# Performance work log

Hardware: AMD Instinct MI355X
Metric: run time of the kernel (lower is better)

## Reference

```python
import jax, jax.numpy as jnp
import numpy as np

N_M = 100000  # musicians
N_T = 100000  # tracks
E = 400000
D = 128


def _sage(x_src, x_dst, edge, W_l, b_l, W_r, n_dst):
    """PyG SAGEConv: lin_l(mean_{j in N(i)} x_src[j]) + lin_r(x_dst[i])."""
    src, dst = edge[0], edge[1]
    msg = x_src[src]                                   # [E, D] gather
    agg = jax.ops.segment_sum(msg, dst, num_segments=n_dst)
    cnt = jax.ops.segment_sum(jnp.ones((edge.shape[1],), x_src.dtype), dst,
                              num_segments=n_dst)
    agg = agg / jnp.maximum(cnt, 1.0)[:, None]         # mean aggregation
    return agg @ W_l.T + b_l + x_dst @ W_r.T


def setup_inputs() -> dict:
    key = jax.random.key(0)
    ks = jax.random.split(key, 7)
    scale = 0.05
    return {
        "x_m": jax.random.normal(ks[0], (N_M, D), jnp.float32),
        "x_t": jax.random.normal(ks[1], (N_T, D), jnp.float32),
        "Wl": jax.random.normal(ks[2], (3, 2, D, D), jnp.float32) * scale,
        "bl": jnp.zeros((3, 2, D), jnp.float32),
        "Wr": jax.random.normal(ks[3], (3, 2, D, D), jnp.float32) * scale,
        "edge_mt": jax.random.randint(ks[4], (2, E), 0, N_T, jnp.int32).astype(jnp.int64),
        "edge_tm": jax.random.randint(ks[5], (2, E), 0, N_M, jnp.int32).astype(jnp.int64),
    }


def reference(x_m, x_t, Wl, bl, Wr, edge_mt, edge_tm):
    # 3 HeteroConv(SAGEConv) layers; dropout=0.0 is identity.
    for layer in range(3):
        # edge type 0: musician -plays_on-> track  (dst = track)
        new_t = _sage(x_m, x_t, edge_mt, Wl[layer, 0], bl[layer, 0], Wr[layer, 0], N_T)
        # edge type 1: track -features-> musician  (dst = musician)
        new_m = _sage(x_t, x_m, edge_tm, Wl[layer, 1], bl[layer, 1], Wr[layer, 1], N_M)
        if layer < 2:
            new_m = jax.nn.relu(new_m)
            new_t = jax.nn.relu(new_t)
        x_m, x_t = new_m, new_t
    return x_m, x_t
```

## Files before the change

### kernel.cpp

```cpp
#include <hip/hip_runtime.h>
#include <hip/hip_bf16.h>

typedef __bf16 bf16_t;
typedef __attribute__((ext_vector_type(4))) __bf16 bf16x4;
typedef __attribute__((ext_vector_type(8))) __bf16 bf16x8;
typedef __attribute__((ext_vector_type(4))) float f32x4;

#define DIM 128

__device__ __forceinline__ void gl_lds16(const void* g, void* l) {
    __builtin_amdgcn_global_load_lds(
        (const __attribute__((address_space(1))) unsigned int*)g,
        (__attribute__((address_space(3))) unsigned int*)l, 16, 0, 0);
}

__global__ void prep_count(const float* __restrict__ Wl, const float* __restrict__ Wr,
                           bf16_t* __restrict__ Wc,
                           const int* __restrict__ dA, int* __restrict__ cA,
                           const int* __restrict__ dB, int* __restrict__ cB,
                           int E, int PB) {
    int blk = blockIdx.x;
    if (blk < PB) {
        int idx = blk * 256 + threadIdx.x;
        if (idx >= 6 * 128 * 256) return;
        int k = idx & 255;
        int n = (idx >> 8) & 127;
        int s = idx >> 15;
        float v;
        if (k < 128) v = Wl[((size_t)s * 128 + n) * 128 + k];
        else         v = Wr[((size_t)s * 128 + n) * 128 + (k - 128)];
        Wc[idx] = (bf16_t)v;
    } else {
        int i = (blk - PB) * 256 + threadIdx.x;
        if (i < E) atomicAdd(&cA[dA[i]], 1);
        else if (i < 2 * E) atomicAdd(&cB[dB[i - E]], 1);
    }
}

__global__ __launch_bounds__(256) void scan_local2(
    const int* __restrict__ cntA, int* __restrict__ partA, int* __restrict__ bsumA,
    int MA, int NBA,
    const int* __restrict__ cntB, int* __restrict__ partB, int* __restrict__ bsumB,
    int MB) {
    int blk = blockIdx.x;
    const int* cnt; int* partial; int* blocksum; int M; int b;
    if (blk < NBA) { cnt = cntA; partial = partA; blocksum = bsumA; M = MA; b = blk; }
    else           { cnt = cntB; partial = partB; blocksum = bsumB; M = MB; b = blk - NBA; }
    __shared__ int sdata[256];
    int i = b * 256 + threadIdx.x;
    int v = (i < M) ? cnt[i] : 0;
    sdata[threadIdx.x] = v;
    __syncthreads();
    for (int off = 1; off < 256; off <<= 1) {
        int t = (threadIdx.x >= off) ? sdata[threadIdx.x - off] : 0;
        __syncthreads();
        sdata[threadIdx.x] += t;
        __syncthreads();
    }
    int incl = sdata[threadIdx.x];
    if (i < M) partial[i] = incl - v;
    if (threadIdx.x == 255) blocksum[b] = incl;
}

__global__ __launch_bounds__(256) void scan_blocks2(int* __restrict__ bsA, int NA,
                                                    int* __restrict__ bsB, int NBcnt) {
    int* blocksum = blockIdx.x ? bsB : bsA;
    int NB = blockIdx.x ? NBcnt : NA;
    __shared__ int sdata[256];
    __shared__ int running;
    if (threadIdx.x == 0) running = 0;
    __syncthreads();
    for (int base = 0; base < NB; base += 256) {
        int i = base + threadIdx.x;
        int v = (i < NB) ? blocksum[i] : 0;
        sdata[threadIdx.x] = v;
        __syncthreads();
        for (int off = 1; off < 256; off <<= 1) {
            int t = (threadIdx.x >= off) ? sdata[threadIdx.x - off] : 0;
            __syncthreads();
            sdata[threadIdx.x] += t;
            __syncthreads();
        }
        int incl = sdata[threadIdx.x];
        int r = running;
        __syncthreads();
        if (i < NB) blocksum[i] = incl - v + r;
        if (threadIdx.x == 0) running = r + sdata[255];
        __syncthreads();
    }
}

__global__ __launch_bounds__(256) void add_offsets2(
    const int* __restrict__ pA, const int* __restrict__ bsA,
    int* __restrict__ rsA, int* __restrict__ curA, int MA, int NBA,
    const int* __restrict__ pB, const int* __restrict__ bsB,
    int* __restrict__ rsB, int* __restrict__ curB, int MB) {
    int blk = blockIdx.x;
    const int *partial, *blocksum; int *rowstart, *cursor; int M, b;
    if (blk < NBA) { partial = pA; blocksum = bsA; rowstart = rsA; cursor = curA; M = MA; b = blk; }
    else           { partial = pB; blocksum = bsB; rowstart = rsB; cursor = curB; M = MB; b = blk - NBA; }
    int i = b * 256 + threadIdx.x;
    if (i < M) {
        int rs = partial[i] + blocksum[i >> 8];
        rowstart[i] = rs;
        cursor[i] = rs;
    }
}

__global__ void bin_edges2(const int* __restrict__ sA, const int* __restrict__ dA,
                           int* __restrict__ curA, int* __restrict__ csrA,
                           const int* __restrict__ sB, const int* __restrict__ dB,
                           int* __restrict__ curB, int* __restrict__ csrB, int E) {
    int e = blockIdx.x * blockDim.x + threadIdx.x;
    if (e < E) {
        int d = dA[e];
        int pos = atomicAdd(&curA[d], 1);
        csrA[pos] = sA[e];
    } else if (e < 2 * E) {
        int i = e - E;
        int d = dB[i];
        int pos = atomicAdd(&curB[d], 1);
        csrB[pos] = sB[i];
    }
}

__global__ __launch_bounds__(256) void gather2(
    const float* __restrict__ xsA, const int* __restrict__ rsA,
    const int* __restrict__ cnA, const int* __restrict__ csA,
    bf16_t* __restrict__ agA, int MA,
    const float* __restrict__ xsB, const int* __restrict__ rsB,
    const int* __restrict__ cnB, const int* __restrict__ csB,
    bf16_t* __restrict__ agB, int MB) {
    int gw   = (blockIdx.x * 256 + threadIdx.x) >> 6;
    int lane = threadIdx.x & 63;
    int half = lane >> 5;
    int l32  = lane & 31;
    int side = gw & 1;
    int d    = (gw >> 1) * 2 + half;
    const float* xs; const int *rs, *cn, *cs; bf16_t* ag; int M;
    if (side == 0) { xs = xsA; rs = rsA; cn = cnA; cs = csA; ag = agA; M = MA; }
    else           { xs = xsB; rs = rsB; cn = cnB; cs = csB; ag = agB; M = MB; }
    if (d >= M) return;

    int start = rs[d];
    int n = cn[d];
    float4 acc0 = {0.f, 0.f, 0.f, 0.f};
    float4 acc1 = {0.f, 0.f, 0.f, 0.f};
    for (int k = 0; k < n; k += 8) {
        int sv[8];
#pragma unroll
        for (int j = 0; j < 8; ++j) {
            int kk = k + j;
            sv[j] = cs[start + min(kk, n - 1)];
        }
        float4 vv[8];
#pragma unroll
        for (int j = 0; j < 8; ++j)
            vv[j] = ((const float4*)(xs + (size_t)sv[j] * DIM))[l32];
#pragma unroll
        for (int j = 0; j < 8; j += 2) {
            float w0 = (k + j     < n) ? 1.f : 0.f;
            float w1 = (k + j + 1 < n) ? 1.f : 0.f;
            acc0.x += vv[j].x * w0; acc0.y += vv[j].y * w0;
            acc0.z += vv[j].z * w0; acc0.w += vv[j].w * w0;
            acc1.x += vv[j + 1].x * w1; acc1.y += vv[j + 1].y * w1;
            acc1.z += vv[j + 1].z * w1; acc1.w += vv[j + 1].w * w1;
        }
    }
    float invn = 1.0f / (float)max(n, 1);
    bf16x4 r;
    r[0] = (bf16_t)((acc0.x + acc1.x) * invn);
    r[1] = (bf16_t)((acc0.y + acc1.y) * invn);
    r[2] = (bf16_t)((acc0.z + acc1.z) * invn);
    r[3] = (bf16_t)((acc0.w + acc1.w) * invn);
    *(bf16x4*)(ag + (size_t)d * DIM + l32 * 4) = r;
}

#define GTILE   32
#define A0BYTES 8192
#define A1BYTES 16384
#define LDSBUF  (A0BYTES + A1BYTES)

template <bool RELU>
__global__ __launch_bounds__(256, 3) void gemm2(
    const bf16_t* __restrict__ A0a, const float* __restrict__ A1a,
    const bf16_t* __restrict__ Wca, const float* __restrict__ ba,
    float* __restrict__ oa, int Ma,
    const bf16_t* __restrict__ A0b, const float* __restrict__ A1b,
    const bf16_t* __restrict__ Wcb, const float* __restrict__ bb,
    float* __restrict__ ob, int Mb) {
    __shared__ char smem[2 * LDSBUF];
    const int tid  = threadIdx.x;
    const int wid  = tid >> 6;
    const int lane = tid & 63;
    const int quad = lane >> 4;
    const int l16  = lane & 15;

    const int side = blockIdx.x & 1;
    const int t0   = blockIdx.x >> 1;
    const int gs   = gridDim.x >> 1;

    const bf16_t* A0; const float* A1; const bf16_t* Wc; const float* bias; float* out; int M;
    if (side == 0) { A0 = A0a; A1 = A1a; Wc = Wca; bias = ba; out = oa; M = Ma; }
    else           { A0 = A0b; A1 = A1b; Wc = Wcb; bias = bb; out = ob; M = Mb; }
    const int nt = (M + GTILE - 1) / GTILE;
    if (t0 >= nt) return;

    bf16x8 breg[2][8];
#pragma unroll
    for (int ct = 0; ct < 2; ++ct)
#pragma unroll
        for (int kt = 0; kt < 8; ++kt)
            breg[ct][kt] = *(const bf16x8*)(
                Wc + (size_t)(wid * 32 + ct * 16 + l16) * 256 + kt * 32 + quad * 8);

    const float bcol0 = bias[wid * 32 + l16];
    const float bcol1 = bias[wid * 32 + 16 + l16];
    const int sw = l16 & 7;

    int a0row[2], a0sc[2];
#pragma unroll
    for (int c = 0; c < 2; ++c) {
        int o  = wid * 2048 + c * 1024 + lane * 16;
        int row = o >> 8;
        int ch  = (o >> 4) & 15;
        a0row[c] = row;
        a0sc[c]  = (ch ^ (row & 7)) * 8;
    }
    int a1row[4], a1sc[4];
#pragma unroll
    for (int c = 0; c < 4; ++c) {
        int o  = wid * 4096 + c * 1024 + lane * 16;
        int row = o >> 9;
        int ch  = (o >> 4) & 31;
        a1row[c] = row;
        a1sc[c]  = (ch ^ (row & 7)) * 4;
    }

    auto STAGE = [&](int b, int t) {
        const int r0 = t * GTILE;
        char* base = smem + b * LDSBUF;
#pragma unroll
        for (int c = 0; c < 2; ++c) {
            int grow = r0 + a0row[c]; if (grow >= M) grow = M - 1;
            gl_lds16(A0 + (size_t)grow * DIM + a0sc[c],
                     base + wid * 2048 + c * 1024);
        }
#pragma unroll
        for (int c = 0; c < 4; ++c) {
            int grow = r0 + a1row[c]; if (grow >= M) grow = M - 1;
            gl_lds16(A1 + (size_t)grow * DIM + a1sc[c],
                     base + A0BYTES + wid * 4096 + c * 1024);
        }
    };

    auto COMPUTE = [&](int b, int t) {
        const int r0 = t * GTILE;
        const char* a0base = smem + b * LDSBUF;
        const char* a1base = a0base + A0BYTES;
        f32x4 acc[2][2];
#pragma unroll
        for (int rt = 0; rt < 2; ++rt) {
            acc[rt][0] = (f32x4){0.f, 0.f, 0.f, 0.f};
            acc[rt][1] = (f32x4){0.f, 0.f, 0.f, 0.f};
        }
#pragma unroll
        for (int rt = 0; rt < 2; ++rt) {
            const int row = rt * 16 + l16;
            bf16x8 alo[4];
#pragma unroll
            for (int kt = 0; kt < 4; ++kt)
                alo[kt] = *(const bf16x8*)(a0base + row * 256 + ((kt * 4 + quad) ^ sw) * 16);
#pragma unroll
            for (int kt = 0; kt < 4; ++kt) {
                acc[rt][0] = __builtin_amdgcn_mfma_f32_16x16x32_bf16(alo[kt], breg[0][kt], acc[rt][0], 0, 0, 0);
                acc[rt][1] = __builtin_amdgcn_mfma_f32_16x16x32_bf16(alo[kt], breg[1][kt], acc[rt][1], 0, 0, 0);
            }
#pragma unroll
            for (int kt = 0; kt < 4; ++kt) {
                const int cc = kt * 8 + quad * 2;
                float4 x0 = *(const float4*)(a1base + row * 512 + ((cc)     ^ sw) * 16);
                float4 x1 = *(const float4*)(a1base + row * 512 + ((cc + 1) ^ sw) * 16);
                bf16x8 ah;
                ah[0] = (bf16_t)x0.x; ah[1] = (bf16_t)x0.y;
                ah[2] = (bf16_t)x0.z; ah[3] = (bf16_t)x0.w;
                ah[4] = (bf16_t)x1.x; ah[5] = (bf16_t)x1.y;
                ah[6] = (bf16_t)x1.z; ah[7] = (bf16_t)x1.w;
                acc[rt][0] = __builtin_amdgcn_mfma_f32_16x16x32_bf16(ah, breg[0][kt + 4], acc[rt][0], 0, 0, 0);
                acc[rt][1] = __builtin_amdgcn_mfma_f32_16x16x32_bf16(ah, breg[1][kt + 4], acc[rt][1], 0, 0, 0);
            }
        }
#pragma unroll
        for (int ct = 0; ct < 2; ++ct) {
            const int col = wid * 32 + ct * 16 + l16;
            const float bv = ct ? bcol1 : bcol0;
#pragma unroll
            for (int rt = 0; rt < 2; ++rt)
#pragma unroll
                for (int r = 0; r < 4; ++r) {
                    int row = r0 + rt * 16 + quad * 4 + r;
                    if (row < M) {
                        float v = acc[rt][ct][r] + bv;
                        if (RELU) v = fmaxf(v, 0.f);
                        out[(size_t)row * DIM + col] = v;
                    }
                }
        }
    };

    STAGE(0, t0);
    int bufi = 0;
    for (int t = t0; t < nt; t += gs, bufi ^= 1) {
        const int nxt = t + gs;
        if (nxt < nt) {
            STAGE(bufi ^ 1, nxt);
            asm volatile("s_waitcnt vmcnt(6)" ::: "memory");
        } else {
            asm volatile("s_waitcnt vmcnt(0)" ::: "memory");
        }
        __builtin_amdgcn_s_barrier();
        COMPUTE(bufi, t);
        __builtin_amdgcn_s_barrier();
        __builtin_amdgcn_sched_barrier(0);
    }
}

extern "C" void kernel_launch(void* const* d_in, const int* in_sizes, int n_in,
                              void* d_out, int out_size, void* d_ws, size_t ws_size,
                              hipStream_t stream) {
    const float* x_m = (const float*)d_in[0];
    const float* x_t = (const float*)d_in[1];
    const float* Wl  = (const float*)d_in[2];
    const float* bl  = (const float*)d_in[3];
    const float* Wr  = (const float*)d_in[4];
    const int* e_mt  = (const int*)d_in[5];
    const int* e_tm  = (const int*)d_in[6];

    const int Mm = in_sizes[0] / DIM;
    const int Mt = in_sizes[1] / DIM;
    const int E  = in_sizes[5] / 2;
    const int NBt = (Mt + 255) / 256;
    const int NBm = (Mm + 255) / 256;

    float* out_m = (float*)d_out;
    float* out_t = (float*)d_out + (size_t)Mm * DIM;

    char* ws = (char*)d_ws;
    size_t off = 0;
    auto alloc = [&](size_t bytes) -> void* {
        void* p = ws + off;
        off += (bytes + 255) & ~(size_t)255;
        return p;
    };
    float*  xm2    = (float*)alloc((size_t)Mm * DIM * 4);
    float*  xt2    = (float*)alloc((size_t)Mt * DIM * 4);
    bf16_t* aggT   = (bf16_t*)alloc((size_t)Mt * DIM * 2);
    bf16_t* aggM   = (bf16_t*)alloc((size_t)Mm * DIM * 2);
    int*    cnt_t  = (int*)alloc((size_t)Mt * 4);
    int*    cnt_m  = (int*)alloc((size_t)Mm * 4);
    int*    rs_t   = (int*)alloc((size_t)Mt * 4);
    int*    rs_m   = (int*)alloc((size_t)Mm * 4);
    int*    cur_tb = (int*)alloc((size_t)Mt * 4);
    int*    cur_mb = (int*)alloc((size_t)Mm * 4);
    int*    part_t = (int*)alloc((size_t)Mt * 4);
    int*    part_m = (int*)alloc((size_t)Mm * 4);
    int*    bsum_t = (int*)alloc((size_t)NBt * 4);
    int*    bsum_m = (int*)alloc((size_t)NBm * 4);
    int*    csr_t  = (int*)alloc((size_t)E * 4);
    int*    csr_m  = (int*)alloc((size_t)E * 4);
    bf16_t* Wc     = (bf16_t*)alloc((size_t)6 * 128 * 256 * 2);

    hipMemsetAsync(cnt_t, 0, (size_t)Mt * 4, stream);
    hipMemsetAsync(cnt_m, 0, (size_t)Mm * 4, stream);

    const int PB = (6 * 128 * 256 + 255) / 256;
    const int CB = (2 * E + 255) / 256;
    prep_count<<<PB + CB, 256, 0, stream>>>(Wl, Wr, Wc, e_mt + E, cnt_t, e_tm + E, cnt_m, E, PB);

    scan_local2<<<NBt + NBm, 256, 0, stream>>>(cnt_t, part_t, bsum_t, Mt, NBt,
                                               cnt_m, part_m, bsum_m, Mm);
    scan_blocks2<<<2, 256, 0, stream>>>(bsum_t, NBt, bsum_m, NBm);
    add_offsets2<<<NBt + NBm, 256, 0, stream>>>(part_t, bsum_t, rs_t, cur_tb, Mt, NBt,
                                                part_m, bsum_m, rs_m, cur_mb, Mm);
    bin_edges2<<<(2 * E + 255) / 256, 256, 0, stream>>>(e_mt, e_mt + E, cur_tb, csr_t,
                                                        e_tm, e_tm + E, cur_mb, csr_m, E);

    const int wT = (Mt + 1) / 2, wM = (Mm + 1) / 2;
    const int gwaves = 2 * ((wT > wM) ? wT : wM);
    const int gblocks = (gwaves + 3) / 4;

    int GG = 768;
    {
        int ntT = (Mt + GTILE - 1) / GTILE, ntM = (Mm + GTILE - 1) / GTILE;
        int need = 2 * ((ntT > ntM) ? ntT : ntM);
        if (GG > need) GG = need;
        GG &= ~1;
        if (GG < 2) GG = 2;
    }

    const float* cm = x_m;
    const float* ct = x_t;
    for (int layer = 0; layer < 3; ++layer) {
        float *nxt_m, *nxt_t;
        if (layer == 1) { nxt_m = xm2;   nxt_t = xt2;   }
        else            { nxt_m = out_m; nxt_t = out_t; }
        const float* biasT = bl + ((size_t)layer * 2 + 0) * DIM;
        const float* biasM = bl + ((size_t)layer * 2 + 1) * DIM;
        const bf16_t* WcT = Wc + ((size_t)layer * 2 + 0) * 128 * 256;
        const bf16_t* WcM = Wc + ((size_t)layer * 2 + 1) * 128 * 256;

        gather2<<<gblocks, 256, 0, stream>>>(cm, rs_t, cnt_t, csr_t, aggT, Mt,
                                             ct, rs_m, cnt_m, csr_m, aggM, Mm);
        if (layer < 2)
            gemm2<true ><<<GG, 256, 0, stream>>>(aggT, ct, WcT, biasT, nxt_t, Mt,
                                                 aggM, cm, WcM, biasM, nxt_m, Mm);
        else
            gemm2<false><<<GG, 256, 0, stream>>>(aggT, ct, WcT, biasT, nxt_t, Mt,
                                                 aggM, cm, WcM, biasM, nxt_m, Mm);

        cm = nxt_m;
        ct = nxt_t;
    }
}
```

Measured before the change: 567.2 us.

## Fuse neighbor-mean gather into the GEMM kernel and store intermediates in bf16

```diff
diff --git a/kernel.cpp b/kernel.cpp
--- a/kernel.cpp
+++ b/kernel.cpp
@@ -7,6 +7,7 @@
 typedef __attribute__((ext_vector_type(4))) float f32x4;
 
 #define DIM 128
+#define GTILE 32
 
 __device__ __forceinline__ void gl_lds16(const void* g, void* l) {
     __builtin_amdgcn_global_load_lds(
@@ -124,72 +125,21 @@
     }
 }
 
-__global__ __launch_bounds__(256) void gather2(
-    const float* __restrict__ xsA, const int* __restrict__ rsA,
+#define A0SZ 8192
+
+template <int MODE>
+__global__ __launch_bounds__(256, 3) void fused2(
+    const void* __restrict__ gsA, const int* __restrict__ rsA,
     const int* __restrict__ cnA, const int* __restrict__ csA,
-    bf16_t* __restrict__ agA, int MA,
-    const float* __restrict__ xsB, const int* __restrict__ rsB,
+    const void* __restrict__ a1A, const bf16_t* __restrict__ WcA,
+    const float* __restrict__ bA, void* __restrict__ oA, int Ma,
+    const void* __restrict__ gsB, const int* __restrict__ rsB,
     const int* __restrict__ cnB, const int* __restrict__ csB,
-    bf16_t* __restrict__ agB, int MB) {
-    int gw   = (blockIdx.x * 256 + threadIdx.x) >> 6;
-    int lane = threadIdx.x & 63;
-    int half = lane >> 5;
-    int l32  = lane & 31;
-    int side = gw & 1;
-    int d    = (gw >> 1) * 2 + half;
-    const float* xs; const int *rs, *cn, *cs; bf16_t* ag; int M;
-    if (side == 0) { xs = xsA; rs = rsA; cn = cnA; cs = csA; ag = agA; M = MA; }
-    else           { xs = xsB; rs = rsB; cn = cnB; cs = csB; ag = agB; M = MB; }
-    if (d >= M) return;
-
-    int start = rs[d];
-    int n = cn[d];
-    float4 acc0 = {0.f, 0.f, 0.f, 0.f};
-    float4 acc1 = {0.f, 0.f, 0.f, 0.f};
-    for (int k = 0; k < n; k += 8) {
-        int sv[8];
-#pragma unroll
-        for (int j = 0; j < 8; ++j) {
-            int kk = k + j;
-            sv[j] = cs[start + min(kk, n - 1)];
-        }
-        float4 vv[8];
-#pragma unroll
-        for (int j = 0; j < 8; ++j)
-            vv[j] = ((const float4*)(xs + (size_t)sv[j] * DIM))[l32];
-#pragma unroll
-        for (int j = 0; j < 8; j += 2) {
-            float w0 = (k + j     < n) ? 1.f : 0.f;
-            float w1 = (k + j + 1 < n) ? 1.f : 0.f;
-            acc0.x += vv[j].x * w0; acc0.y += vv[j].y * w0;
-            acc0.z += vv[j].z * w0; acc0.w += vv[j].w * w0;
-            acc1.x += vv[j + 1].x * w1; acc1.y += vv[j + 1].y * w1;
-            acc1.z += vv[j + 1].z * w1; acc1.w += vv[j + 1].w * w1;
-        }
-    }
-    float invn = 1.0f / (float)max(n, 1);
-    bf16x4 r;
-    r[0] = (bf16_t)((acc0.x + acc1.x) * invn);
-    r[1] = (bf16_t)((acc0.y + acc1.y) * invn);
-    r[2] = (bf16_t)((acc0.z + acc1.z) * invn);
-    r[3] = (bf16_t)((acc0.w + acc1.w) * invn);
-    *(bf16x4*)(ag + (size_t)d * DIM + l32 * 4) = r;
-}
-
-#define GTILE   32
-#define A0BYTES 8192
-#define A1BYTES 16384
-#define LDSBUF  (A0BYTES + A1BYTES)
-
-template <bool RELU>
-__global__ __launch_bounds__(256, 3) void gemm2(
-    const bf16_t* __restrict__ A0a, const float* __restrict__ A1a,
-    const bf16_t* __restrict__ Wca, const float* __restrict__ ba,
-    float* __restrict__ oa, int Ma,
-    const bf16_t* __restrict__ A0b, const float* __restrict__ A1b,
-    const bf16_t* __restrict__ Wcb, const float* __restrict__ bb,
-    float* __restrict__ ob, int Mb) {
-    __shared__ char smem[2 * LDSBUF];
+    const void* __restrict__ a1B, const bf16_t* __restrict__ WcB,
+    const float* __restrict__ bB, void* __restrict__ oB, int Mb) {
+    constexpr int A1SZ = (MODE == 0) ? 16384 : 8192;
+    __shared__ char smem[A0SZ + 2 * A1SZ];
+
     const int tid  = threadIdx.x;
     const int wid  = tid >> 6;
     const int lane = tid & 63;
@@ -200,9 +150,12 @@
     const int t0   = blockIdx.x >> 1;
     const int gs   = gridDim.x >> 1;
 
-    const bf16_t* A0; const float* A1; const bf16_t* Wc; const float* bias; float* out; int M;
-    if (side == 0) { A0 = A0a; A1 = A1a; Wc = Wca; bias = ba; out = oa; M = Ma; }
-    else           { A0 = A0b; A1 = A1b; Wc = Wcb; bias = bb; out = ob; M = Mb; }
+    const void *gsrc, *a1p; const int *rsx, *cnx, *csx;
+    const bf16_t* Wc; const float* bias; void* outp; int M;
+    if (side == 0) { gsrc = gsA; rsx = rsA; cnx = cnA; csx = csA; a1p = a1A;
+                     Wc = WcA; bias = bA; outp = oA; M = Ma; }
+    else           { gsrc = gsB; rsx = rsB; cnx = cnB; csx = csB; a1p = a1B;
+                     Wc = WcB; bias = bB; outp = oB; M = Mb; }
     const int nt = (M + GTILE - 1) / GTILE;
     if (t0 >= nt) return;
 
@@ -218,46 +171,108 @@
     const float bcol1 = bias[wid * 32 + 16 + l16];
     const int sw = l16 & 7;
 
-    int a0row[2], a0sc[2];
-#pragma unroll
-    for (int c = 0; c < 2; ++c) {
-        int o  = wid * 2048 + c * 1024 + lane * 16;
-        int row = o >> 8;
-        int ch  = (o >> 4) & 15;
-        a0row[c] = row;
-        a0sc[c]  = (ch ^ (row & 7)) * 8;
-    }
-    int a1row[4], a1sc[4];
-#pragma unroll
-    for (int c = 0; c < 4; ++c) {
-        int o  = wid * 4096 + c * 1024 + lane * 16;
-        int row = o >> 9;
-        int ch  = (o >> 4) & 31;
-        a1row[c] = row;
-        a1sc[c]  = (ch ^ (row & 7)) * 4;
+    int s_row[4], s_off[4];
+    if constexpr (MODE == 0) {
+#pragma unroll
+        for (int c = 0; c < 4; ++c) {
+            int o = wid * 4096 + c * 1024 + lane * 16;
+            int row = o >> 9;
+            int ch  = (o >> 4) & 31;
+            s_row[c] = row;
+            s_off[c] = (ch ^ (row & 7)) * 4;
+        }
+    } else {
+#pragma unroll
+        for (int c = 0; c < 2; ++c) {
+            int o = wid * 2048 + c * 1024 + lane * 16;
+            int row = o >> 8;
+            int ch  = (o >> 4) & 15;
+            s_row[c] = row;
+            s_off[c] = (ch ^ (row & 7)) * 8;
+        }
     }
 
     auto STAGE = [&](int b, int t) {
         const int r0 = t * GTILE;
-        char* base = smem + b * LDSBUF;
-#pragma unroll
-        for (int c = 0; c < 2; ++c) {
-            int grow = r0 + a0row[c]; if (grow >= M) grow = M - 1;
-            gl_lds16(A0 + (size_t)grow * DIM + a0sc[c],
-                     base + wid * 2048 + c * 1024);
-        }
-#pragma unroll
-        for (int c = 0; c < 4; ++c) {
-            int grow = r0 + a1row[c]; if (grow >= M) grow = M - 1;
-            gl_lds16(A1 + (size_t)grow * DIM + a1sc[c],
-                     base + A0BYTES + wid * 4096 + c * 1024);
+        char* base = smem + A0SZ + b * A1SZ;
+        if constexpr (MODE == 0) {
+            const float* A1f = (const float*)a1p;
+#pragma unroll
+            for (int c = 0; c < 4; ++c) {
+                int grow = r0 + s_row[c]; if (grow >= M) grow = M - 1;
+                gl_lds16(A1f + (size_t)grow * DIM + s_off[c],
+                         base + wid * 4096 + c * 1024);
+            }
+        } else {
+            const bf16_t* A1h = (const bf16_t*)a1p;
+#pragma unroll
+            for (int c = 0; c < 2; ++c) {
+                int grow = r0 + s_row[c]; if (grow >= M) grow = M - 1;
+                gl_lds16(A1h + (size_t)grow * DIM + s_off[c],
+                         base + wid * 2048 + c * 1024);
+            }
+        }
+    };
+
+    auto GATHER = [&](int t) {
+        const int hw  = tid >> 5;
+        const int l32 = tid & 31;
+        char* a0 = smem;
+#pragma unroll 1
+        for (int rr = 0; rr < 4; ++rr) {
+            int r = hw * 4 + rr;
+            int d = t * GTILE + r;
+            float4 acc0 = {0.f, 0.f, 0.f, 0.f};
+            float4 acc1 = {0.f, 0.f, 0.f, 0.f};
+            int n = 0;
+            if (d < M) {
+                int start = rsx[d];
+                n = cnx[d];
+                for (int k = 0; k < n; k += 8) {
+                    int sv[8];
+#pragma unroll
+                    for (int j = 0; j < 8; ++j)
+                        sv[j] = csx[start + min(k + j, n - 1)];
+                    float4 vv[8];
+                    if constexpr (MODE == 0) {
+                        const float* xg = (const float*)gsrc;
+#pragma unroll
+                        for (int j = 0; j < 8; ++j)
+                            vv[j] = ((const float4*)(xg + (size_t)sv[j] * DIM))[l32];
+                    } else {
+                        const bf16_t* xg = (const bf16_t*)gsrc;
+#pragma unroll
+                        for (int j = 0; j < 8; ++j) {
+                            bf16x4 b4 = *(const bf16x4*)(xg + (size_t)sv[j] * DIM + l32 * 4);
+                            vv[j] = (float4){(float)b4[0], (float)b4[1],
+                                             (float)b4[2], (float)b4[3]};
+                        }
+                    }
+#pragma unroll
+                    for (int j = 0; j < 8; j += 2) {
+                        float w0 = (k + j     < n) ? 1.f : 0.f;
+                        float w1 = (k + j + 1 < n) ? 1.f : 0.f;
+                        acc0.x += vv[j].x * w0; acc0.y += vv[j].y * w0;
+                        acc0.z += vv[j].z * w0; acc0.w += vv[j].w * w0;
+                        acc1.x += vv[j + 1].x * w1; acc1.y += vv[j + 1].y * w1;
+                        acc1.z += vv[j + 1].z * w1; acc1.w += vv[j + 1].w * w1;
+                    }
+                }
+            }
+            float invn = 1.0f / (float)max(n, 1);
+            bf16x4 res;
+            res[0] = (bf16_t)((acc0.x + acc1.x) * invn);
+            res[1] = (bf16_t)((acc0.y + acc1.y) * invn);
+            res[2] = (bf16_t)((acc0.z + acc1.z) * invn);
+            res[3] = (bf16_t)((acc0.w + acc1.w) * invn);
+            *(bf16x4*)(a0 + r * 256 + (((l32 >> 1) ^ (r & 7)) << 4) + ((l32 & 1) << 3)) = res;
         }
     };
 
     auto COMPUTE = [&](int b, int t) {
         const int r0 = t * GTILE;
-        const char* a0base = smem + b * LDSBUF;
-        const char* a1base = a0base + A0BYTES;
+        const char* a0base = smem;
+        const char* a1base = smem + A0SZ + b * A1SZ;
         f32x4 acc[2][2];
 #pragma unroll
         for (int rt = 0; rt < 2; ++rt) {
@@ -276,18 +291,27 @@
                 acc[rt][0] = __builtin_amdgcn_mfma_f32_16x16x32_bf16(alo[kt], breg[0][kt], acc[rt][0], 0, 0, 0);
                 acc[rt][1] = __builtin_amdgcn_mfma_f32_16x16x32_bf16(alo[kt], breg[1][kt], acc[rt][1], 0, 0, 0);
             }
-#pragma unroll
-            for (int kt = 0; kt < 4; ++kt) {
-                const int cc = kt * 8 + quad * 2;
-                float4 x0 = *(const float4*)(a1base + row * 512 + ((cc)     ^ sw) * 16);
-                float4 x1 = *(const float4*)(a1base + row * 512 + ((cc + 1) ^ sw) * 16);
-                bf16x8 ah;
-                ah[0] = (bf16_t)x0.x; ah[1] = (bf16_t)x0.y;
-                ah[2] = (bf16_t)x0.z; ah[3] = (bf16_t)x0.w;
-                ah[4] = (bf16_t)x1.x; ah[5] = (bf16_t)x1.y;
-                ah[6] = (bf16_t)x1.z; ah[7] = (bf16_t)x1.w;
-                acc[rt][0] = __builtin_amdgcn_mfma_f32_16x16x32_bf16(ah, breg[0][kt + 4], acc[rt][0], 0, 0, 0);
-                acc[rt][1] = __builtin_amdgcn_mfma_f32_16x16x32_bf16(ah, breg[1][kt + 4], acc[rt][1], 0, 0, 0);
+            if constexpr (MODE == 0) {
+#pragma unroll
+                for (int kt = 0; kt < 4; ++kt) {
+                    const int cc = kt * 8 + quad * 2;
+                    float4 x0 = *(const float4*)(a1base + row * 512 + ((cc)     ^ sw) * 16);
+                    float4 x1 = *(const float4*)(a1base + row * 512 + ((cc + 1) ^ sw) * 16);
+                    bf16x8 ah;
+                    ah[0] = (bf16_t)x0.x; ah[1] = (bf16_t)x0.y;
+                    ah[2] = (bf16_t)x0.z; ah[3] = (bf16_t)x0.w;
+                    ah[4] = (bf16_t)x1.x; ah[5] = (bf16_t)x1.y;
+                    ah[6] = (bf16_t)x1.z; ah[7] = (bf16_t)x1.w;
+                    acc[rt][0] = __builtin_amdgcn_mfma_f32_16x16x32_bf16(ah, breg[0][kt + 4], acc[rt][0], 0, 0, 0);
+                    acc[rt][1] = __builtin_amdgcn_mfma_f32_16x16x32_bf16(ah, breg[1][kt + 4], acc[rt][1], 0, 0, 0);
+                }
+            } else {
+#pragma unroll
+                for (int kt = 0; kt < 4; ++kt) {
+                    bf16x8 ah = *(const bf16x8*)(a1base + row * 256 + ((kt * 4 + quad) ^ sw) * 16);
+                    acc[rt][0] = __builtin_amdgcn_mfma_f32_16x16x32_bf16(ah, breg[0][kt + 4], acc[rt][0], 0, 0, 0);
+                    acc[rt][1] = __builtin_amdgcn_mfma_f32_16x16x32_bf16(ah, breg[1][kt + 4], acc[rt][1], 0, 0, 0);
+                }
             }
         }
 #pragma unroll
@@ -301,27 +325,25 @@
                     int row = r0 + rt * 16 + quad * 4 + r;
                     if (row < M) {
                         float v = acc[rt][ct][r] + bv;
-                        if (RELU) v = fmaxf(v, 0.f);
-                        out[(size_t)row * DIM + col] = v;
+                        if (MODE < 2) v = fmaxf(v, 0.f);
+                        if constexpr (MODE == 2)
+                            ((float*)outp)[(size_t)row * DIM + col] = v;
+                        else
+                            ((bf16_t*)outp)[(size_t)row * DIM + col] = (bf16_t)v;
                     }
                 }
         }
     };
 
     STAGE(0, t0);
-    int bufi = 0;
-    for (int t = t0; t < nt; t += gs, bufi ^= 1) {
+    int cur = 0;
+    for (int t = t0; t < nt; t += gs, cur ^= 1) {
         const int nxt = t + gs;
-        if (nxt < nt) {
-            STAGE(bufi ^ 1, nxt);
-            asm volatile("s_waitcnt vmcnt(6)" ::: "memory");
-        } else {
-            asm volatile("s_waitcnt vmcnt(0)" ::: "memory");
-        }
-        __builtin_amdgcn_s_barrier();
-        COMPUTE(bufi, t);
-        __builtin_amdgcn_s_barrier();
-        __builtin_amdgcn_sched_barrier(0);
+        if (nxt < nt) STAGE(cur ^ 1, nxt);
+        GATHER(t);
+        __syncthreads();
+        COMPUTE(cur, t);
+        __syncthreads();
     }
 }
 
@@ -352,10 +374,10 @@
         off += (bytes + 255) & ~(size_t)255;
         return p;
     };
-    float*  xm2    = (float*)alloc((size_t)Mm * DIM * 4);
-    float*  xt2    = (float*)alloc((size_t)Mt * DIM * 4);
-    bf16_t* aggT   = (bf16_t*)alloc((size_t)Mt * DIM * 2);
-    bf16_t* aggM   = (bf16_t*)alloc((size_t)Mm * DIM * 2);
+    bf16_t* xb_m0  = (bf16_t*)alloc((size_t)Mm * DIM * 2);
+    bf16_t* xb_t0  = (bf16_t*)alloc((size_t)Mt * DIM * 2);
+    bf16_t* xb_m1  = (bf16_t*)alloc((size_t)Mm * DIM * 2);
+    bf16_t* xb_t1  = (bf16_t*)alloc((size_t)Mt * DIM * 2);
     int*    cnt_t  = (int*)alloc((size_t)Mt * 4);
     int*    cnt_m  = (int*)alloc((size_t)Mm * 4);
     int*    rs_t   = (int*)alloc((size_t)Mt * 4);
@@ -385,10 +407,6 @@
     bin_edges2<<<(2 * E + 255) / 256, 256, 0, stream>>>(e_mt, e_mt + E, cur_tb, csr_t,
                                                         e_tm, e_tm + E, cur_mb, csr_m, E);
 
-    const int wT = (Mt + 1) / 2, wM = (Mm + 1) / 2;
-    const int gwaves = 2 * ((wT > wM) ? wT : wM);
-    const int gblocks = (gwaves + 3) / 4;
-
     int GG = 768;
     {
         int ntT = (Mt + GTILE - 1) / GTILE, ntM = (Mm + GTILE - 1) / GTILE;
@@ -398,27 +416,20 @@
         if (GG < 2) GG = 2;
     }
 
-    const float* cm = x_m;
-    const float* ct = x_t;
-    for (int layer = 0; layer < 3; ++layer) {
-        float *nxt_m, *nxt_t;
-        if (layer == 1) { nxt_m = xm2;   nxt_t = xt2;   }
-        else            { nxt_m = out_m; nxt_t = out_t; }
-        const float* biasT = bl + ((size_t)layer * 2 + 0) * DIM;
-        const float* biasM = bl + ((size_t)layer * 2 + 1) * DIM;
-        const bf16_t* WcT = Wc + ((size_t)layer * 2 + 0) * 128 * 256;
-        const bf16_t* WcM = Wc + ((size_t)layer * 2 + 1) * 128 * 256;
-
-        gather2<<<gblocks, 256, 0, stream>>>(cm, rs_t, cnt_t, csr_t, aggT, Mt,
-                                             ct, rs_m, cnt_m, csr_m, aggM, Mm);
-        if (layer < 2)
-            gemm2<true ><<<GG, 256, 0, stream>>>(aggT, ct, WcT, biasT, nxt_t, Mt,
-                                                 aggM, cm, WcM, biasM, nxt_m, Mm);
-        else
-            gemm2<false><<<GG, 256, 0, stream>>>(aggT, ct, WcT, biasT, nxt_t, Mt,
-                                                 aggM, cm, WcM, biasM, nxt_m, Mm);
-
-        cm = nxt_m;
-        ct = nxt_t;
-    }
-}
+    const float* biasT0 = bl + 0 * DIM;  const float* biasM0 = bl + 1 * DIM;
+    const float* biasT1 = bl + 2 * DIM;  const float* biasM1 = bl + 3 * DIM;
+    const float* biasT2 = bl + 4 * DIM;  const float* biasM2 = bl + 5 * DIM;
+    const bf16_t* WcT0 = Wc + 0 * 128 * 256;  const bf16_t* WcM0 = Wc + 1 * 128 * 256;
+    const bf16_t* WcT1 = Wc + 2 * 128 * 256;  const bf16_t* WcM1 = Wc + 3 * 128 * 256;
+    const bf16_t* WcT2 = Wc + 4 * 128 * 256;  const bf16_t* WcM2 = Wc + 5 * 128 * 256;
+
+    fused2<0><<<GG, 256, 0, stream>>>(
+        x_m, rs_t, cnt_t, csr_t, x_t, WcT0, biasT0, xb_t0, Mt,
+        x_t, rs_m, cnt_m, csr_m, x_m, WcM0, biasM0, xb_m0, Mm);
+    fused2<1><<<GG, 256, 0, stream>>>(
+        xb_m0, rs_t, cnt_t, csr_t, xb_t0, WcT1, biasT1, xb_t1, Mt,
+        xb_t0, rs_m, cnt_m, csr_m, xb_m0, WcM1, biasM1, xb_m1, Mm);
+    fused2<2><<<GG, 256, 0, stream>>>(
+        xb_m1, rs_t, cnt_t, csr_t, xb_t1, WcT2, biasT2, out_t, Mt,
+        xb_t1, rs_m, cnt_m, csr_m, xb_m1, WcM2, biasM2, out_m, Mm);
+}
```

Result: faster. 511.4 us (-9.8%).
